# Kernel tuning notes

Measured on AMD Instinct MI355X. Metric: run time of the kernel, lower is better.

The kernel has to match this reference:

```python
import jax, jax.numpy as jnp
import numpy as np


def setup_inputs() -> dict:
    key = jax.random.key(0)
    k1, k2 = jax.random.split(key)
    B, H, W, D, C = 4, 128, 128, 128, 2
    image = jax.random.normal(k1, (B, H, W, D, C), dtype=jnp.float32)
    # near-identity affine so sampling is meaningful (localization-net output stand-in)
    theta = 0.1 * jax.random.normal(k2, (B, 3, 4), dtype=jnp.float32) + jnp.eye(3, 4, dtype=jnp.float32)[None]
    return {"image": image, "theta": theta}


def reference(image, theta):
    # Faithful port of SpatialTransformer._transform / _interpolate (incl. its
    # original index-flattening and z-weight (z1 - z0) conventions).
    B, H, W, D, C = image.shape
    oH, oW, oD = H, W, D  # downsample_factor = 1
    N = oH * oW * oD

    # _meshgrid: tf.meshgrid default 'xy' indexing -> shapes (oH, oW, oD)
    xl = jnp.linspace(-1.0, 1.0, oW)
    yl = jnp.linspace(-1.0, 1.0, oH)
    zl = jnp.linspace(-1.0, 1.0, oD)
    Xg, Yg, Zg = jnp.meshgrid(xl, yl, zl)
    grid = jnp.stack([Xg.ravel(), Yg.ravel(), Zg.ravel(), jnp.ones(N, jnp.float32)], 0)  # [4, N]

    tg = jnp.einsum('bij,jn->bin', theta.astype(jnp.float32), grid)  # [B, 3, N]
    x = tg[:, 0, :].reshape(-1)
    y = tg[:, 1, :].reshape(-1)
    z = tg[:, 2, :].reshape(-1)

    # map from [-1, 1] to pixel coords (original uses full extent, not extent-1)
    x = 0.5 * (x + 1.0) * W
    y = 0.5 * (y + 1.0) * H
    z = 0.5 * (z + 1.0) * D

    x0 = jnp.floor(x).astype(jnp.int32); x1 = x0 + 1
    y0 = jnp.floor(y).astype(jnp.int32); y1 = y0 + 1
    z0 = jnp.floor(z).astype(jnp.int32); z1 = z0 + 1
    x0 = jnp.clip(x0, 0, W - 1); x1 = jnp.clip(x1, 0, W - 1)
    y0 = jnp.clip(y0, 0, H - 1); y1 = jnp.clip(y1, 0, H - 1)
    z0 = jnp.clip(z0, 0, D - 1); z1 = jnp.clip(z1, 0, D - 1)

    base = jnp.repeat(jnp.arange(B, dtype=jnp.int32) * (H * W * D), N)  # [B*N]
    # original flat-index convention: base + y*W + z*W*H + x
    b00 = base + y0 * W + z0 * (W * H)
    b10 = base + y1 * W + z0 * (W * H)
    b01 = base + y0 * W + z1 * (W * H)
    b11 = base + y1 * W + z1 * (W * H)

    flat = image.reshape(-1, C).astype(jnp.float32)  # [B*H*W*D, C]
    pa = flat[b00 + x0]; pb = flat[b10 + x0]
    pc = flat[b00 + x1]; pd = flat[b10 + x1]
    pe = flat[b01 + x0]; pf = flat[b11 + x0]
    pg = flat[b01 + x1]; ph = flat[b11 + x1]

    x0f = x0.astype(jnp.float32); x1f = x1.astype(jnp.float32)
    y0f = y0.astype(jnp.float32); y1f = y1.astype(jnp.float32)
    z0f = z0.astype(jnp.float32); z1f = z1.astype(jnp.float32)

    wa = ((x1f - x) * (y1f - y) * (z1f - z))[:, None]
    wb = ((x1f - x) * (y - y0f) * (z1f - z))[:, None]
    wc = ((x - x0f) * (y1f - y) * (z1f - z))[:, None]
    wd = ((x - x0f) * (y - y0f) * (z1f - z))[:, None]
    we = ((x1f - x) * (y1f - y) * (z1f - z0f))[:, None]
    wf = ((x1f - x) * (y - y0f) * (z1f - z0f))[:, None]
    wg = ((x - x0f) * (y1f - y) * (z1f - z0f))[:, None]
    wh = ((x - x0f) * (y - y0f) * (z1f - z0f))[:, None]

    out = (wa * pa + wb * pb + wc * pc + wd * pd
           + we * pe + wf * pf + wg * pg + wh * ph)  # [B*N, C]
    return out.reshape(B, oH, oW, oD, C)
```

## Files before the change

kernel.cpp:

```cpp
#include <hip/hip_runtime.h>
#include <math.h>

#define BN 4
#define HN 128
#define WN 128
#define DN 128

__global__ __launch_bounds__(256) void st_trilerp_kernel(
    const float* __restrict__ image,
    const float* __restrict__ theta,
    float* __restrict__ out)
{
    const int bi = blockIdx.z;
    const int b  = bi >> 7;
    const int i  = bi & (HN - 1);
    const int j0 = blockIdx.y << 4;
    const int k0 = blockIdx.x << 4;

    const int tid = threadIdx.x;
    const int jj = tid & 15;
    const int kk = tid >> 4;
    const int j = j0 + jj;
    const int k = k0 + kk;

    const double step = 2.0 / 127.0;
    const double X = (j == WN - 1) ? 1.0 : (double)j * step - 1.0;
    const double Y = (i == HN - 1) ? 1.0 : (double)i * step - 1.0;
    const double Z = (k == DN - 1) ? 1.0 : (double)k * step - 1.0;

    const float* th = theta + b * 12;
    const double xt = (((double)th[0] * X + (double)th[1] * Y) + (double)th[2]  * Z) + (double)th[3];
    const double yt = (((double)th[4] * X + (double)th[5] * Y) + (double)th[6]  * Z) + (double)th[7];
    const double zt = (((double)th[8] * X + (double)th[9] * Y) + (double)th[10] * Z) + (double)th[11];

    const double x = (0.5 * (xt + 1.0)) * (double)WN;
    const double y = (0.5 * (yt + 1.0)) * (double)HN;
    const double z = (0.5 * (zt + 1.0)) * (double)DN;

    const int x0u = (int)floor(x);
    const int y0u = (int)floor(y);
    const int z0u = (int)floor(z);
    const int x0 = min(max(x0u,     0), WN - 1);
    const int x1 = min(max(x0u + 1, 0), WN - 1);
    const int y0 = min(max(y0u,     0), HN - 1);
    const int y1 = min(max(y0u + 1, 0), HN - 1);
    const int z0 = min(max(z0u,     0), DN - 1);
    const int z1 = min(max(z0u + 1, 0), DN - 1);

    const int base = b * (HN * WN * DN);
    const int b00 = base + y0 * WN + z0 * (WN * HN);
    const int b10 = base + y1 * WN + z0 * (WN * HN);
    const int b01 = base + y0 * WN + z1 * (WN * HN);
    const int b11 = base + y1 * WN + z1 * (WN * HN);

    const float2* __restrict__ img2 = (const float2*)image;

    const int xb = min(x0, WN - 2);
    const bool lo0 = (x0 == xb);
    const bool lo1 = (x1 == xb);

    const float4 q00 = *(const float4*)(img2 + b00 + xb);
    const float4 q10 = *(const float4*)(img2 + b10 + xb);
    const float4 q01 = *(const float4*)(img2 + b01 + xb);
    const float4 q11 = *(const float4*)(img2 + b11 + xb);

    const float2 pa = lo0 ? make_float2(q00.x, q00.y) : make_float2(q00.z, q00.w);
    const float2 pc = lo1 ? make_float2(q00.x, q00.y) : make_float2(q00.z, q00.w);
    const float2 pb = lo0 ? make_float2(q10.x, q10.y) : make_float2(q10.z, q10.w);
    const float2 pd = lo1 ? make_float2(q10.x, q10.y) : make_float2(q10.z, q10.w);
    const float2 pe = lo0 ? make_float2(q01.x, q01.y) : make_float2(q01.z, q01.w);
    const float2 pg = lo1 ? make_float2(q01.x, q01.y) : make_float2(q01.z, q01.w);
    const float2 pf = lo0 ? make_float2(q11.x, q11.y) : make_float2(q11.z, q11.w);
    const float2 ph = lo1 ? make_float2(q11.x, q11.y) : make_float2(q11.z, q11.w);

    const float wx0 = (float)((double)x1 - x), wx1 = (float)(x - (double)x0);
    const float wy0 = (float)((double)y1 - y), wy1 = (float)(y - (double)y0);
    const float wz0 = (float)((double)z1 - z);
    const float wzA = (float)(z1 - z0);

    const float wa = wx0 * wy0 * wz0;
    const float wb = wx0 * wy1 * wz0;
    const float wc = wx1 * wy0 * wz0;
    const float wd = wx1 * wy1 * wz0;
    const float we = wx0 * wy0 * wzA;
    const float wf = wx0 * wy1 * wzA;
    const float wg = wx1 * wy0 * wzA;
    const float wh = wx1 * wy1 * wzA;

    float2 o;
    o.x = wa * pa.x + wb * pb.x + wc * pc.x + wd * pd.x
        + we * pe.x + wf * pf.x + wg * pg.x + wh * ph.x;
    o.y = wa * pa.y + wb * pb.y + wc * pc.y + wd * pd.y
        + we * pe.y + wf * pf.y + wg * pg.y + wh * ph.y;

    __shared__ float2 tile[16][17];
    tile[kk][jj] = o;
    __syncthreads();

    const int kw = tid & 15;
    const int jw = tid >> 4;
    const int oidx = (bi * WN + (j0 + jw)) * DN + (k0 + kw);
    ((float2*)out)[oidx] = tile[kw][jw];
}

extern "C" void kernel_launch(void* const* d_in, const int* in_sizes, int n_in,
                              void* d_out, int out_size, void* d_ws, size_t ws_size,
                              hipStream_t stream) {
    const float* image = (const float*)d_in[0];
    const float* theta = (const float*)d_in[1];
    float* out = (float*)d_out;

    dim3 grid(DN / 16, WN / 16, BN * HN);
    st_trilerp_kernel<<<grid, 256, 0, stream>>>(image, theta, out);
}
```

Measured before the change: 145.0 us.

## Compute four output voxels per thread with affine-incremental coords and direct vector stores

Each thread now produces four consecutive k outputs. The affine transform is folded into a per-thread linear function of k, which reduces double-precision work per voxel. Weights are factored into separable x/y/z lerps, and the shared-memory transpose and barrier are dropped in favour of direct float4 stores of the four results. The cost is more registers per thread and fewer blocks, and the store pattern changes: each thread writes 32 contiguous bytes, strided by j across the wavefront. Changing the interpolation's floating-point order may cause small rounding differences.

Result: slower. 158.8 us (+9.5%).

```diff
diff --git a/kernel.cpp b/kernel.cpp
--- a/kernel.cpp
+++ b/kernel.cpp
@@ -15,92 +15,94 @@
     const int b  = bi >> 7;
     const int i  = bi & (HN - 1);
     const int j0 = blockIdx.y << 4;
-    const int k0 = blockIdx.x << 4;
+    const int k0 = blockIdx.x << 6;
 
     const int tid = threadIdx.x;
-    const int jj = tid & 15;
-    const int kk = tid >> 4;
-    const int j = j0 + jj;
-    const int k = k0 + kk;
+    const int jj  = tid & 15;
+    const int kt  = tid >> 4;
+    const int j   = j0 + jj;
+    const int kb  = k0 + (kt << 2);
 
     const double step = 2.0 / 127.0;
     const double X = (j == WN - 1) ? 1.0 : (double)j * step - 1.0;
     const double Y = (i == HN - 1) ? 1.0 : (double)i * step - 1.0;
-    const double Z = (k == DN - 1) ? 1.0 : (double)k * step - 1.0;
 
     const float* th = theta + b * 12;
-    const double xt = (((double)th[0] * X + (double)th[1] * Y) + (double)th[2]  * Z) + (double)th[3];
-    const double yt = (((double)th[4] * X + (double)th[5] * Y) + (double)th[6]  * Z) + (double)th[7];
-    const double zt = (((double)th[8] * X + (double)th[9] * Y) + (double)th[10] * Z) + (double)th[11];
+    const double t0 = (double)th[0], t1 = (double)th[1], t2  = (double)th[2],  t3  = (double)th[3];
+    const double t4 = (double)th[4], t5 = (double)th[5], t6  = (double)th[6],  t7  = (double)th[7];
+    const double t8 = (double)th[8], t9 = (double)th[9], t10 = (double)th[10], t11 = (double)th[11];
 
-    const double x = (0.5 * (xt + 1.0)) * (double)WN;
-    const double y = (0.5 * (yt + 1.0)) * (double)HN;
-    const double z = (0.5 * (zt + 1.0)) * (double)DN;
-
-    const int x0u = (int)floor(x);
-    const int y0u = (int)floor(y);
-    const int z0u = (int)floor(z);
-    const int x0 = min(max(x0u,     0), WN - 1);
-    const int x1 = min(max(x0u + 1, 0), WN - 1);
-    const int y0 = min(max(y0u,     0), HN - 1);
-    const int y1 = min(max(y0u + 1, 0), HN - 1);
-    const int z0 = min(max(z0u,     0), DN - 1);
-    const int z1 = min(max(z0u + 1, 0), DN - 1);
+    const double KST = 128.0 / 127.0;
+    const double Px = t2  * KST, Qx = fma(64.0, (t0*X + t1*Y) + t3  - t2,  64.0);
+    const double Py = t6  * KST, Qy = fma(64.0, (t4*X + t5*Y) + t7  - t6,  64.0);
+    const double Pz = t10 * KST, Qz = fma(64.0, (t8*X + t9*Y) + t11 - t10, 64.0);
 
     const int base = b * (HN * WN * DN);
-    const int b00 = base + y0 * WN + z0 * (WN * HN);
-    const int b10 = base + y1 * WN + z0 * (WN * HN);
-    const int b01 = base + y0 * WN + z1 * (WN * HN);
-    const int b11 = base + y1 * WN + z1 * (WN * HN);
-
     const float2* __restrict__ img2 = (const float2*)image;
 
-    const int xb = min(x0, WN - 2);
-    const bool lo0 = (x0 == xb);
-    const bool lo1 = (x1 == xb);
+    float4 q00[4], q10[4], q01[4], q11[4];
+    float  wxL[4], wxH[4], wy0[4], wy1[4], wz0[4], wzA[4];
 
-    const float4 q00 = *(const float4*)(img2 + b00 + xb);
-    const float4 q10 = *(const float4*)(img2 + b10 + xb);
-    const float4 q01 = *(const float4*)(img2 + b01 + xb);
-    const float4 q11 = *(const float4*)(img2 + b11 + xb);
+#pragma unroll
+    for (int c = 0; c < 4; ++c) {
+        const double kd = (double)(kb + c);
+        const double x = fma(Px, kd, Qx);
+        const double y = fma(Py, kd, Qy);
+        const double z = fma(Pz, kd, Qz);
 
-    const float2 pa = lo0 ? make_float2(q00.x, q00.y) : make_float2(q00.z, q00.w);
-    const float2 pc = lo1 ? make_float2(q00.x, q00.y) : make_float2(q00.z, q00.w);
-    const float2 pb = lo0 ? make_float2(q10.x, q10.y) : make_float2(q10.z, q10.w);
-    const float2 pd = lo1 ? make_float2(q10.x, q10.y) : make_float2(q10.z, q10.w);
-    const float2 pe = lo0 ? make_float2(q01.x, q01.y) : make_float2(q01.z, q01.w);
-    const float2 pg = lo1 ? make_float2(q01.x, q01.y) : make_float2(q01.z, q01.w);
-    const float2 pf = lo0 ? make_float2(q11.x, q11.y) : make_float2(q11.z, q11.w);
-    const float2 ph = lo1 ? make_float2(q11.x, q11.y) : make_float2(q11.z, q11.w);
+        const double xf = floor(x), yf = floor(y), zf = floor(z);
+        const int x0u = (int)xf, y0u = (int)yf, z0u = (int)zf;
+        const int x0 = min(max(x0u,     0), WN - 1);
+        const int x1 = min(max(x0u + 1, 0), WN - 1);
+        const int y0 = min(max(y0u,     0), HN - 1);
+        const int y1 = min(max(y0u + 1, 0), HN - 1);
+        const int z0 = min(max(z0u,     0), DN - 1);
+        const int z1 = min(max(z0u + 1, 0), DN - 1);
 
-    const float wx0 = (float)((double)x1 - x), wx1 = (float)(x - (double)x0);
-    const float wy0 = (float)((double)y1 - y), wy1 = (float)(y - (double)y0);
-    const float wz0 = (float)((double)z1 - z);
-    const float wzA = (float)(z1 - z0);
+        const float xs = (float)x, ys = (float)y, zs = (float)z;
+        const float wx0f = (float)x1 - xs, wx1f = xs - (float)x0;
+        wy0[c] = (float)y1 - ys;  wy1[c] = ys - (float)y0;
+        wz0[c] = (float)z1 - zs;  wzA[c] = (float)(z1 - z0);
 
-    const float wa = wx0 * wy0 * wz0;
-    const float wb = wx0 * wy1 * wz0;
-    const float wc = wx1 * wy0 * wz0;
-    const float wd = wx1 * wy1 * wz0;
-    const float we = wx0 * wy0 * wzA;
-    const float wf = wx0 * wy1 * wzA;
-    const float wg = wx1 * wy0 * wzA;
-    const float wh = wx1 * wy1 * wzA;
+        const int xb  = min(x0, WN - 2);
+        const bool lo0 = (x0 == xb), lo1 = (x1 == xb);
+        wxL[c] = (lo0 ? wx0f : 0.0f) + (lo1 ? wx1f : 0.0f);
+        wxH[c] = (lo0 ? 0.0f : wx0f) + (lo1 ? 0.0f : wx1f);
 
-    float2 o;
-    o.x = wa * pa.x + wb * pb.x + wc * pc.x + wd * pd.x
-        + we * pe.x + wf * pf.x + wg * pg.x + wh * ph.x;
-    o.y = wa * pa.y + wb * pb.y + wc * pc.y + wd * pd.y
-        + we * pe.y + wf * pf.y + wg * pg.y + wh * ph.y;
+        const int r00 = base + (y0 << 7) + (z0 << 14) + xb;
+        const int dy  = (y1 - y0) << 7;
+        const int dz  = (z1 - z0) << 14;
+        q00[c] = *(const float4*)(img2 + r00);
+        q10[c] = *(const float4*)(img2 + r00 + dy);
+        q01[c] = *(const float4*)(img2 + r00 + dz);
+        q11[c] = *(const float4*)(img2 + r00 + dy + dz);
+    }
 
-    __shared__ float2 tile[16][17];
-    tile[kk][jj] = o;
-    __syncthreads();
+    float ox[4], oy[4];
+#pragma unroll
+    for (int c = 0; c < 4; ++c) {
+        const float g00x = wxL[c]*q00[c].x + wxH[c]*q00[c].z;
+        const float g00y = wxL[c]*q00[c].y + wxH[c]*q00[c].w;
+        const float g10x = wxL[c]*q10[c].x + wxH[c]*q10[c].z;
+        const float g10y = wxL[c]*q10[c].y + wxH[c]*q10[c].w;
+        const float g01x = wxL[c]*q01[c].x + wxH[c]*q01[c].z;
+        const float g01y = wxL[c]*q01[c].y + wxH[c]*q01[c].w;
+        const float g11x = wxL[c]*q11[c].x + wxH[c]*q11[c].z;
+        const float g11y = wxL[c]*q11[c].y + wxH[c]*q11[c].w;
 
-    const int kw = tid & 15;
-    const int jw = tid >> 4;
-    const int oidx = (bi * WN + (j0 + jw)) * DN + (k0 + kw);
-    ((float2*)out)[oidx] = tile[kw][jw];
+        const float h0x = wy0[c]*g00x + wy1[c]*g10x;
+        const float h0y = wy0[c]*g00y + wy1[c]*g10y;
+        const float h1x = wy0[c]*g01x + wy1[c]*g11x;
+        const float h1y = wy0[c]*g01y + wy1[c]*g11y;
+
+        ox[c] = wz0[c]*h0x + wzA[c]*h1x;
+        oy[c] = wz0[c]*h0y + wzA[c]*h1y;
+    }
+
+    const int oidx = (bi * WN + j) * DN + kb;
+    float4* op = (float4*)((float2*)out + oidx);
+    op[0] = make_float4(ox[0], oy[0], ox[1], oy[1]);
+    op[1] = make_float4(ox[2], oy[2], ox[3], oy[3]);
 }
 
 extern "C" void kernel_launch(void* const* d_in, const int* in_sizes, int n_in,
@@ -110,6 +112,6 @@
     const float* theta = (const float*)d_in[1];
     float* out = (float*)d_out;
 
-    dim3 grid(DN / 16, WN / 16, BN * HN);
+    dim3 grid(DN / 64, WN / 16, BN * HN);
     st_trilerp_kernel<<<grid, 256, 0, stream>>>(image, theta, out);
 }
```
